# Kernel tuning notes

Hardware: AMD Instinct MI355X
Metric: run time of the kernel (lower is better)

Reference implementation:

```python
import jax, jax.numpy as jnp
import numpy as np

B, CIN, COUT, H, W, HEADS = 8, 128, 128, 256, 256, 32
CI = COUT // HEADS  # channels per head


def setup_inputs() -> dict:
    key = jax.random.key(0)
    ks = jax.random.split(key, 6)
    s_in = (2.0 / CIN) ** 0.5
    s_mid = (2.0 / COUT) ** 0.5
    return {
        "u": jax.random.normal(ks[0], (B, CIN, H, W), jnp.float32),
        "w_f1": jax.random.normal(ks[1], (COUT, CIN), jnp.float32) * s_in,
        "b_f1": jnp.zeros((COUT,), jnp.float32),
        # small flow weights -> small displacements (realistic warping)
        "w_f2": jax.random.normal(ks[2], (2 * HEADS, COUT), jnp.float32) * 0.02 * s_mid,
        "b_f2": jnp.zeros((2 * HEADS,), jnp.float32),
        "w_v": jax.random.normal(ks[3], (COUT, CIN), jnp.float32) * s_in,
        "b_v": jnp.zeros((COUT,), jnp.float32),
    }


def _conv1x1(x, w, b):
    # x: (B, Cin, H, W), w: (Cout, Cin) -> (B, Cout, H, W)
    return jnp.einsum('bchw,oc->bohw', x, w) + b[None, :, None, None]


def _periodic_bilinear(v, grid):
    """grid_sample, bilinear, align_corners=False, periodic in both H and W.
    Equivalent to custom_grid_sample2d with padding_modes=('periodic','periodic'):
    pixel coords are wrapped mod size and the (i+1) neighbor wraps to index 0
    (the torch code pads with the first row/col and samples with border mode).
    v: (N, C, H, W); grid: (N, H, W, 2) with [...,0]=x, [...,1]=y in [-1,1].
    """
    N, C, Hi, Wi = v.shape
    gx, gy = grid[..., 0], grid[..., 1]
    # unnormalize (align_corners=False) then wrap periodically
    px = jnp.mod(((gx + 1.0) * Wi - 1.0) * 0.5, Wi)
    py = jnp.mod(((gy + 1.0) * Hi - 1.0) * 0.5, Hi)
    x0 = jnp.floor(px)
    y0 = jnp.floor(py)
    wx = px - x0
    wy = py - y0
    x0i = jnp.clip(x0.astype(jnp.int32), 0, Wi - 1)
    y0i = jnp.clip(y0.astype(jnp.int32), 0, Hi - 1)
    x1i = jnp.mod(x0i + 1, Wi)
    y1i = jnp.mod(y0i + 1, Hi)
    vf = v.reshape(N, C, Hi * Wi)

    def gather(yi, xi):
        idx = (yi * Wi + xi).reshape(N, 1, Hi * Wi)
        return jnp.take_along_axis(vf, idx, axis=2).reshape(N, C, Hi, Wi)

    w00 = ((1.0 - wx) * (1.0 - wy))[:, None]
    w01 = (wx * (1.0 - wy))[:, None]
    w10 = ((1.0 - wx) * wy)[:, None]
    w11 = (wx * wy)[:, None]
    return (gather(y0i, x0i) * w00 + gather(y0i, x1i) * w01
            + gather(y1i, x0i) * w10 + gather(y1i, x1i) * w11)


def _base_grid(Hi, Wi):
    # create_grid: stack(meshgrid[::-1]) -> [...,0]=x (varies along W), [...,1]=y
    yy, xx = jnp.meshgrid(jnp.linspace(-1.0, 1.0, Hi),
                          jnp.linspace(-1.0, 1.0, Wi), indexing='ij')
    return jnp.stack([xx, yy], axis=-1)  # (H, W, 2)


def reference(u, w_f1, b_f1, w_f2, b_f2, w_v, b_v):
    Bq = u.shape[0]
    # flow_head: conv1x1 -> relu -> conv1x1
    hmid = jax.nn.relu(_conv1x1(u, w_f1, b_f1))
    flow = _conv1x1(hmid, w_f2, b_f2)          # (B, heads*2, H, W)
    value = _conv1x1(u, w_v, b_v)              # (B, Cout, H, W)
    # rearrange 'B (heads dir) H W -> (B heads) H W dir'
    flow = flow.reshape(Bq, HEADS, 2, H, W).transpose(0, 1, 3, 4, 2)
    flow = flow.reshape(Bq * HEADS, H, W, 2)
    grid = _base_grid(H, W)[None] + flow       # warp: x + delta(x)
    # rearrange 'B (heads C_i) H W -> (B heads) C_i H W'
    vh = value.reshape(Bq * HEADS, CI, H, W)
    out = _periodic_bilinear(vh, grid)
    # '(B heads) C_i H W -> B (heads C_i) H W'
    return out.reshape(Bq, COUT, H, W)
```

## Files before the change

### kernel.cpp

```cpp
#include <hip/hip_runtime.h>
#include <hip/hip_fp16.h>


typedef unsigned short u16;
typedef unsigned int   u32;
using short8   = __attribute__((ext_vector_type(8))) short;
using f32x4    = __attribute__((ext_vector_type(4))) float;
using ushort4v = __attribute__((ext_vector_type(4))) unsigned short;

#define HW     65536
#define NTILES 8192

__device__ __forceinline__ u16 f2h(float f) {
  return __half_as_ushort(__float2half(f));
}
__device__ __forceinline__ float h2f(u16 h) {
  return __half2float(__ushort_as_half(h));
}

#define BAR_LGKM() do {                                      \
    asm volatile("s_waitcnt lgkmcnt(0)" ::: "memory");       \
    __builtin_amdgcn_s_barrier();                            \
    asm volatile("" ::: "memory");                           \
  } while (0)

__device__ __forceinline__ short8 frag_from_f32(const float* __restrict__ src) {
  float4 a = *(const float4*)src;
  float4 b = *(const float4*)(src + 4);
  short8 r;
  r[0] = (short)f2h(a.x); r[1] = (short)f2h(a.y);
  r[2] = (short)f2h(a.z); r[3] = (short)f2h(a.w);
  r[4] = (short)f2h(b.x); r[5] = (short)f2h(b.y);
  r[6] = (short)f2h(b.z); r[7] = (short)f2h(b.w);
  return r;
}

__device__ __forceinline__ void vf_load_tile(const float* __restrict__ u,
                                             int tile, int tid,
                                             float* __restrict__ r) {
  const int gbase = tile << 6;
  const float* ub = u + ((size_t)(gbase >> 16) << 23) + (gbase & 65535);
  const int p  = tid & 63;
  const int cb = (tid >> 6) << 3;
#pragma unroll
  for (int pass = 0; pass < 4; ++pass)
#pragma unroll
    for (int j = 0; j < 8; ++j)
      r[pass * 8 + j] = ub[(size_t)(cb + pass * 32 + j) * HW + p];
}

__device__ __forceinline__ void vf_write_tile(u16* __restrict__ buf, int tid,
                                              const float* __restrict__ r) {
  const int p  = tid & 63;
  const int cb = (tid >> 6) << 3;
#pragma unroll
  for (int pass = 0; pass < 4; ++pass) {
    int c0 = cb + pass * 32;
    uint4 pk;
    pk.x = (u32)f2h(r[pass * 8 + 0]) | ((u32)f2h(r[pass * 8 + 1]) << 16);
    pk.y = (u32)f2h(r[pass * 8 + 2]) | ((u32)f2h(r[pass * 8 + 3]) << 16);
    pk.z = (u32)f2h(r[pass * 8 + 4]) | ((u32)f2h(r[pass * 8 + 5]) << 16);
    pk.w = (u32)f2h(r[pass * 8 + 6]) | ((u32)f2h(r[pass * 8 + 7]) << 16);
    *(uint4*)((char*)buf + p * 256 + (((c0 >> 3) ^ (p & 15)) << 4)) = pk;
  }
}

__global__ __launch_bounds__(256, 2) void vf_kernel(
    const float* __restrict__ u,  const float* __restrict__ w1,
    const float* __restrict__ b1, const float* __restrict__ w2,
    const float* __restrict__ b2, const float* __restrict__ wv,
    const float* __restrict__ bv, u16* __restrict__ vout,
    u32* __restrict__ fout)
{
  __shared__ u16 t_lds[2][64 * 128];

  const int tid  = threadIdx.x;
  const int lane = tid & 63;
  const int w    = tid >> 6;
  const int m15  = lane & 15;
  const int q    = lane >> 4;

  short8 w1f[2][4], wvf[2][4], w2f[4];
#pragma unroll
  for (int nt = 0; nt < 2; ++nt)
#pragma unroll
    for (int kc = 0; kc < 4; ++kc) {
      const int row = w * 32 + nt * 16 + m15;
      w1f[nt][kc] = frag_from_f32(w1 + row * 128 + kc * 32 + q * 8);
      wvf[nt][kc] = frag_from_f32(wv + row * 128 + kc * 32 + q * 8);
    }
#pragma unroll
  for (int kc = 0; kc < 4; ++kc)
    w2f[kc] = frag_from_f32(w2 + (w * 16 + m15) * 128 + kc * 32 + q * 8);

  f32x4 vbias[2], hbias[2], fbias;
#pragma unroll
  for (int nt = 0; nt < 2; ++nt) {
    vbias[nt] = *(const f32x4*)(bv + w * 32 + nt * 16 + q * 4);
    hbias[nt] = *(const f32x4*)(b1 + w * 32 + nt * 16 + q * 4);
  }
  fbias = *(const f32x4*)(b2 + w * 16 + q * 4);

  const int step = (int)gridDim.x;
  int tile = blockIdx.x;
  float sreg[32];

  vf_load_tile(u, tile, tid, sreg);
  vf_write_tile(t_lds[0], tid, sreg);
  BAR_LGKM();

  int cur = 0;
  for (; tile < NTILES; ) {
    const int gbase = tile << 6;
    const int b     = gbase >> 16;
    const int img   = gbase & 65535;
    const int nxt   = tile + step;
    const bool have_next = (nxt < NTILES);

    if (have_next) vf_load_tile(u, nxt, tid, sreg);

    f32x4 zero = {0.f, 0.f, 0.f, 0.f};
    f32x4 hm[2][4], va[2][4];
#pragma unroll
    for (int nt = 0; nt < 2; ++nt)
#pragma unroll
      for (int pxb = 0; pxb < 4; ++pxb) { hm[nt][pxb] = zero; va[nt][pxb] = zero; }

#pragma unroll
    for (int kc = 0; kc < 4; ++kc) {
      short8 uf[4];
#pragma unroll
      for (int pxb = 0; pxb < 4; ++pxb)
        uf[pxb] = *(const short8*)((const char*)t_lds[cur] +
                                   (pxb * 16 + m15) * 256 +
                                   ((((kc << 2) + q) ^ m15) << 4));
#pragma unroll
      for (int pxb = 0; pxb < 4; ++pxb)
#pragma unroll
        for (int nt = 0; nt < 2; ++nt) {
          hm[nt][pxb] = __builtin_amdgcn_mfma_f32_16x16x32_f16(
              w1f[nt][kc], uf[pxb], hm[nt][pxb], 0, 0, 0);
          va[nt][pxb] = __builtin_amdgcn_mfma_f32_16x16x32_f16(
              wvf[nt][kc], uf[pxb], va[nt][pxb], 0, 0, 0);
        }
    }
    BAR_LGKM();

#pragma unroll
    for (int nt = 0; nt < 2; ++nt) {
      const int ch0   = w * 32 + nt * 16 + q * 4;
      const int chunk = ch0 >> 3;
      const int inner = (ch0 & 7) << 1;
#pragma unroll
      for (int pxb = 0; pxb < 4; ++pxb) {
        const int px = pxb * 16 + m15;
        float h0 = fmaxf(hm[nt][pxb][0] + hbias[nt][0], 0.f);
        float h1 = fmaxf(hm[nt][pxb][1] + hbias[nt][1], 0.f);
        float h2 = fmaxf(hm[nt][pxb][2] + hbias[nt][2], 0.f);
        float h3 = fmaxf(hm[nt][pxb][3] + hbias[nt][3], 0.f);
        uint2 pk;
        pk.x = (u32)f2h(h0) | ((u32)f2h(h1) << 16);
        pk.y = (u32)f2h(h2) | ((u32)f2h(h3) << 16);
        *(uint2*)((char*)t_lds[cur] + px * 256 + ((chunk ^ (px & 15)) << 4) +
                  inner) = pk;
      }
    }

#pragma unroll
    for (int nt = 0; nt < 2; ++nt) {
      const int head = w * 8 + nt * 4 + q;
#pragma unroll
      for (int pxb = 0; pxb < 4; ++pxb) {
        f32x4 v = va[nt][pxb];
        uint2 pk;
        pk.x = (u32)f2h(v[0] + vbias[nt][0]) | ((u32)f2h(v[1] + vbias[nt][1]) << 16);
        pk.y = (u32)f2h(v[2] + vbias[nt][2]) | ((u32)f2h(v[3] + vbias[nt][3]) << 16);
        *(uint2*)(vout + ((((size_t)(b * 32 + head)) << 16) + img +
                          pxb * 16 + m15) * 4) = pk;
      }
    }
    BAR_LGKM();

    f32x4 fl[4];
#pragma unroll
    for (int pxb = 0; pxb < 4; ++pxb) fl[pxb] = zero;
#pragma unroll
    for (int kc = 0; kc < 4; ++kc)
#pragma unroll
      for (int pxb = 0; pxb < 4; ++pxb) {
        short8 hf = *(const short8*)((const char*)t_lds[cur] +
                                     (pxb * 16 + m15) * 256 +
                                     ((((kc << 2) + q) ^ m15) << 4));
        fl[pxb] = __builtin_amdgcn_mfma_f32_16x16x32_f16(
            w2f[kc], hf, fl[pxb], 0, 0, 0);
      }

#pragma unroll
    for (int pxb = 0; pxb < 4; ++pxb) {
      f32x4 v = fl[pxb];
      const int h0 = w * 8 + q * 2;
      u32 pa = (u32)f2h(v[0] + fbias[0]) | ((u32)f2h(v[1] + fbias[1]) << 16);
      u32 pb = (u32)f2h(v[2] + fbias[2]) | ((u32)f2h(v[3] + fbias[3]) << 16);
      u32* fp = fout + (((size_t)(b * 32 + h0)) << 16) + img + pxb * 16 + m15;
      fp[0]  = pa;
      fp[HW] = pb;
    }

    if (have_next) vf_write_tile(t_lds[cur ^ 1], tid, sreg);
    BAR_LGKM();
    cur ^= 1;
    tile = nxt;
  }
}

__global__ __launch_bounds__(256) void warp_kernel(
    const u16* __restrict__ value, const u32* __restrict__ flow,
    float* __restrict__ out)
{
  const int P   = blockIdx.x;
  const int L   = ((P & 7) << 11) | (P >> 3);
  const int hb  = L >> 6;
  const int g   = L & 63;
  const int col = threadIdx.x;

  const u16* vb = value + ((size_t)hb << 18);
  const u32* fp = flow + ((size_t)hb << 16) + (g << 10) + col;

  u32 f[4];
#pragma unroll
  for (int r = 0; r < 4; ++r) f[r] = fp[r << 8];

  float w00[4], w01[4], w10[4], w11[4];
  ushort4v t00[4], t01[4], t10[4], t11[4];
#pragma unroll
  for (int r = 0; r < 4; ++r) {
    float fx = h2f((u16)(f[r] & 0xffffu));
    float fy = h2f((u16)(f[r] >> 16));
    const int hq = (g << 2) + r;
    float gx = -1.f + (2.f / 255.f) * (float)col + fx;
    float gy = -1.f + (2.f / 255.f) * (float)hq + fy;
    float pxr = ((gx + 1.f) * 256.f - 1.f) * 0.5f;
    float pyr = ((gy + 1.f) * 256.f - 1.f) * 0.5f;
    float px = pxr - floorf(pxr * (1.f / 256.f)) * 256.f;
    float py = pyr - floorf(pyr * (1.f / 256.f)) * 256.f;
    if (px >= 256.f) px -= 256.f;
    if (py >= 256.f) py -= 256.f;
    if (px < 0.f) px = 0.f;
    if (py < 0.f) py = 0.f;
    float x0f = floorf(px), y0f = floorf(py);
    float wx = px - x0f, wy = py - y0f;
    int x0 = (int)x0f; if (x0 > 255) x0 = 255;
    int y0 = (int)y0f; if (y0 > 255) y0 = 255;
    int x1 = (x0 + 1) & 255;
    int y1 = (y0 + 1) & 255;
    w00[r] = (1.f - wx) * (1.f - wy);
    w01[r] = wx * (1.f - wy);
    w10[r] = (1.f - wx) * wy;
    w11[r] = wx * wy;
    t00[r] = *(const ushort4v*)(vb + ((y0 * 256 + x0) << 2));
    t01[r] = *(const ushort4v*)(vb + ((y0 * 256 + x1) << 2));
    t10[r] = *(const ushort4v*)(vb + ((y1 * 256 + x0) << 2));
    t11[r] = *(const ushort4v*)(vb + ((y1 * 256 + x1) << 2));
  }

  float* ob = out + ((size_t)hb << 18) + (g << 10) + col;
#pragma unroll
  for (int r = 0; r < 4; ++r)
#pragma unroll
    for (int ci = 0; ci < 4; ++ci) {
      float res = w00[r] * h2f(t00[r][ci]) + w01[r] * h2f(t01[r][ci])
                + w10[r] * h2f(t10[r][ci]) + w11[r] * h2f(t11[r][ci]);
      __builtin_nontemporal_store(res, ob + (r << 8) + ((size_t)ci << 16));
    }
}

extern "C" void kernel_launch(void* const* d_in, const int* in_sizes, int n_in,
                              void* d_out, int out_size, void* d_ws, size_t ws_size,
                              hipStream_t stream) {
  const float* u  = (const float*)d_in[0];
  const float* w1 = (const float*)d_in[1];
  const float* b1 = (const float*)d_in[2];
  const float* w2 = (const float*)d_in[3];
  const float* b2 = (const float*)d_in[4];
  const float* wv = (const float*)d_in[5];
  const float* bv = (const float*)d_in[6];

  u16* value_ws = (u16*)d_ws;
  u32* flow_ws  = (u32*)((char*)d_ws + 134217728);
  float* out    = (float*)d_out;

  vf_kernel<<<dim3(512), dim3(256), 0, stream>>>(u, w1, b1, w2, b2, wv, bv,
                                                 value_ws, flow_ws);
  warp_kernel<<<dim3(16384), dim3(256), 0, stream>>>(value_ws, flow_ws, out);
}
```

Before: 766.7 us.

## Stream input tiles via global_load_lds double buffer and coarsen warp kernel rows

The value/flow kernel now prefetches the next input tile straight into an fp32 LDS double buffer with global_load_lds. It then converts that buffer to an fp16 tile in a separate step, which frees the 32 staging registers and takes the global-load latency off the register path. The warp kernel now handles 8 rows per block instead of 4, in two batches of gathers, and folds the grid unnormalization into one fma. The cost is more LDS per block, which may limit occupancy, and an extra barrier per tile.

```diff
diff --git a/kernel.cpp b/kernel.cpp
--- a/kernel.cpp
+++ b/kernel.cpp
@@ -35,33 +35,38 @@
   return r;
 }
 
-__device__ __forceinline__ void vf_load_tile(const float* __restrict__ u,
-                                             int tile, int tid,
-                                             float* __restrict__ r) {
+__device__ __forceinline__ void vf_issue_tile(const float* __restrict__ u,
+                                              int tile, int tid,
+                                              float* __restrict__ sbuf) {
   const int gbase = tile << 6;
-  const float* ub = u + ((size_t)(gbase >> 16) << 23) + (gbase & 65535);
+  const int wave  = tid >> 6;
+  const int lane  = tid & 63;
+  const float* ub = u + ((size_t)(gbase >> 16) << 23) + (gbase & 65535)
+                      + (size_t)(lane >> 4) * HW + ((lane & 15) << 2);
+#pragma unroll
+  for (int i = 0; i < 8; ++i) {
+    const int ch0 = wave * 32 + i * 4;
+    __builtin_amdgcn_global_load_lds(
+        (const __attribute__((address_space(1))) void*)(ub + (size_t)ch0 * HW),
+        (__attribute__((address_space(3))) void*)(sbuf + ch0 * 64),
+        16, 0, 0);
+  }
+}
+
+__device__ __forceinline__ void vf_convert(const float* __restrict__ sbuf,
+                                           u16* __restrict__ T, int tid) {
   const int p  = tid & 63;
   const int cb = (tid >> 6) << 3;
 #pragma unroll
-  for (int pass = 0; pass < 4; ++pass)
-#pragma unroll
-    for (int j = 0; j < 8; ++j)
-      r[pass * 8 + j] = ub[(size_t)(cb + pass * 32 + j) * HW + p];
-}
-
-__device__ __forceinline__ void vf_write_tile(u16* __restrict__ buf, int tid,
-                                              const float* __restrict__ r) {
-  const int p  = tid & 63;
-  const int cb = (tid >> 6) << 3;
-#pragma unroll
   for (int pass = 0; pass < 4; ++pass) {
-    int c0 = cb + pass * 32;
+    const int c0 = cb + pass * 32;
+    const float* rp = sbuf + c0 * 64 + p;
     uint4 pk;
-    pk.x = (u32)f2h(r[pass * 8 + 0]) | ((u32)f2h(r[pass * 8 + 1]) << 16);
-    pk.y = (u32)f2h(r[pass * 8 + 2]) | ((u32)f2h(r[pass * 8 + 3]) << 16);
-    pk.z = (u32)f2h(r[pass * 8 + 4]) | ((u32)f2h(r[pass * 8 + 5]) << 16);
-    pk.w = (u32)f2h(r[pass * 8 + 6]) | ((u32)f2h(r[pass * 8 + 7]) << 16);
-    *(uint4*)((char*)buf + p * 256 + (((c0 >> 3) ^ (p & 15)) << 4)) = pk;
+    pk.x = (u32)f2h(rp[0])   | ((u32)f2h(rp[64])  << 16);
+    pk.y = (u32)f2h(rp[128]) | ((u32)f2h(rp[192]) << 16);
+    pk.z = (u32)f2h(rp[256]) | ((u32)f2h(rp[320]) << 16);
+    pk.w = (u32)f2h(rp[384]) | ((u32)f2h(rp[448]) << 16);
+    *(uint4*)((char*)T + p * 256 + (((c0 >> 3) ^ (p & 15)) << 4)) = pk;
   }
 }
 
@@ -72,7 +77,8 @@
     const float* __restrict__ bv, u16* __restrict__ vout,
     u32* __restrict__ fout)
 {
-  __shared__ u16 t_lds[2][64 * 128];
+  __shared__ float S[2][128 * 64];
+  __shared__ u16   T[64 * 128];
 
   const int tid  = threadIdx.x;
   const int lane = tid & 63;
@@ -102,22 +108,30 @@
   fbias = *(const f32x4*)(b2 + w * 16 + q * 4);
 
   const int step = (int)gridDim.x;
-  int tile = blockIdx.x;
-  float sreg[32];
-
-  vf_load_tile(u, tile, tid, sreg);
-  vf_write_tile(t_lds[0], tid, sreg);
-  BAR_LGKM();
-
-  int cur = 0;
-  for (; tile < NTILES; ) {
+  float* Sc = &S[0][0];
+  float* Sn = &S[1][0];
+
+  vf_issue_tile(u, blockIdx.x, tid, Sc);
+
+  for (int tile = blockIdx.x; tile < NTILES; tile += step) {
     const int gbase = tile << 6;
     const int b     = gbase >> 16;
     const int img   = gbase & 65535;
     const int nxt   = tile + step;
     const bool have_next = (nxt < NTILES);
 
-    if (have_next) vf_load_tile(u, nxt, tid, sreg);
+    if (have_next) vf_issue_tile(u, nxt, tid, Sn);
+
+    if (have_next) {
+      asm volatile("s_waitcnt vmcnt(8)" ::: "memory");
+    } else {
+      asm volatile("s_waitcnt vmcnt(0)" ::: "memory");
+    }
+    __builtin_amdgcn_s_barrier();
+    __builtin_amdgcn_sched_barrier(0);
+
+    vf_convert(Sc, T, tid);
+    BAR_LGKM();
 
     f32x4 zero = {0.f, 0.f, 0.f, 0.f};
     f32x4 hm[2][4], va[2][4];
@@ -131,8 +145,7 @@
       short8 uf[4];
 #pragma unroll
       for (int pxb = 0; pxb < 4; ++pxb)
-        uf[pxb] = *(const short8*)((const char*)t_lds[cur] +
-                                   (pxb * 16 + m15) * 256 +
+        uf[pxb] = *(const short8*)((const char*)T + (pxb * 16 + m15) * 256 +
                                    ((((kc << 2) + q) ^ m15) << 4));
 #pragma unroll
       for (int pxb = 0; pxb < 4; ++pxb)
@@ -161,8 +174,7 @@
         uint2 pk;
         pk.x = (u32)f2h(h0) | ((u32)f2h(h1) << 16);
         pk.y = (u32)f2h(h2) | ((u32)f2h(h3) << 16);
-        *(uint2*)((char*)t_lds[cur] + px * 256 + ((chunk ^ (px & 15)) << 4) +
-                  inner) = pk;
+        *(uint2*)((char*)T + px * 256 + ((chunk ^ (px & 15)) << 4) + inner) = pk;
       }
     }
 
@@ -188,8 +200,7 @@
     for (int kc = 0; kc < 4; ++kc)
 #pragma unroll
       for (int pxb = 0; pxb < 4; ++pxb) {
-        short8 hf = *(const short8*)((const char*)t_lds[cur] +
-                                     (pxb * 16 + m15) * 256 +
+        short8 hf = *(const short8*)((const char*)T + (pxb * 16 + m15) * 256 +
                                      ((((kc << 2) + q) ^ m15) << 4));
         fl[pxb] = __builtin_amdgcn_mfma_f32_16x16x32_f16(
             w2f[kc], hf, fl[pxb], 0, 0, 0);
@@ -206,10 +217,7 @@
       fp[HW] = pb;
     }
 
-    if (have_next) vf_write_tile(t_lds[cur ^ 1], tid, sreg);
-    BAR_LGKM();
-    cur ^= 1;
-    tile = nxt;
+    float* t = Sc; Sc = Sn; Sn = t;
   }
 }
 
@@ -218,60 +226,65 @@
     float* __restrict__ out)
 {
   const int P   = blockIdx.x;
-  const int L   = ((P & 7) << 11) | (P >> 3);
-  const int hb  = L >> 6;
-  const int g   = L & 63;
+  const int L   = ((P & 7) << 10) | (P >> 3);
+  const int hb  = L >> 5;
+  const int g   = L & 31;
   const int col = threadIdx.x;
 
   const u16* vb = value + ((size_t)hb << 18);
-  const u32* fp = flow + ((size_t)hb << 16) + (g << 10) + col;
-
-  u32 f[4];
-#pragma unroll
-  for (int r = 0; r < 4; ++r) f[r] = fp[r << 8];
-
-  float w00[4], w01[4], w10[4], w11[4];
-  ushort4v t00[4], t01[4], t10[4], t11[4];
-#pragma unroll
-  for (int r = 0; r < 4; ++r) {
-    float fx = h2f((u16)(f[r] & 0xffffu));
-    float fy = h2f((u16)(f[r] >> 16));
-    const int hq = (g << 2) + r;
-    float gx = -1.f + (2.f / 255.f) * (float)col + fx;
-    float gy = -1.f + (2.f / 255.f) * (float)hq + fy;
-    float pxr = ((gx + 1.f) * 256.f - 1.f) * 0.5f;
-    float pyr = ((gy + 1.f) * 256.f - 1.f) * 0.5f;
-    float px = pxr - floorf(pxr * (1.f / 256.f)) * 256.f;
-    float py = pyr - floorf(pyr * (1.f / 256.f)) * 256.f;
-    if (px >= 256.f) px -= 256.f;
-    if (py >= 256.f) py -= 256.f;
-    if (px < 0.f) px = 0.f;
-    if (py < 0.f) py = 0.f;
-    float x0f = floorf(px), y0f = floorf(py);
-    float wx = px - x0f, wy = py - y0f;
-    int x0 = (int)x0f; if (x0 > 255) x0 = 255;
-    int y0 = (int)y0f; if (y0 > 255) y0 = 255;
-    int x1 = (x0 + 1) & 255;
-    int y1 = (y0 + 1) & 255;
-    w00[r] = (1.f - wx) * (1.f - wy);
-    w01[r] = wx * (1.f - wy);
-    w10[r] = (1.f - wx) * wy;
-    w11[r] = wx * wy;
-    t00[r] = *(const ushort4v*)(vb + ((y0 * 256 + x0) << 2));
-    t01[r] = *(const ushort4v*)(vb + ((y0 * 256 + x1) << 2));
-    t10[r] = *(const ushort4v*)(vb + ((y1 * 256 + x0) << 2));
-    t11[r] = *(const ushort4v*)(vb + ((y1 * 256 + x1) << 2));
-  }
-
-  float* ob = out + ((size_t)hb << 18) + (g << 10) + col;
-#pragma unroll
-  for (int r = 0; r < 4; ++r)
-#pragma unroll
-    for (int ci = 0; ci < 4; ++ci) {
-      float res = w00[r] * h2f(t00[r][ci]) + w01[r] * h2f(t01[r][ci])
-                + w10[r] * h2f(t10[r][ci]) + w11[r] * h2f(t11[r][ci]);
-      __builtin_nontemporal_store(res, ob + (r << 8) + ((size_t)ci << 16));
-    }
+  const u32* fp = flow + ((size_t)hb << 16) + (g << 11) + col;
+
+  u32 f[8];
+#pragma unroll
+  for (int r = 0; r < 8; ++r) f[r] = fp[r << 8];
+
+  const float cbase = (float)col * (256.f / 255.f) - 0.5f;
+  float* ob = out + ((size_t)hb << 18) + (g << 11) + col;
+
+#pragma unroll
+  for (int half = 0; half < 2; ++half) {
+    float w00[4], w01[4], w10[4], w11[4];
+    ushort4v t00[4], t01[4], t10[4], t11[4];
+#pragma unroll
+    for (int j = 0; j < 4; ++j) {
+      const int r  = half * 4 + j;
+      const int hq = (g << 3) + r;
+      float fx = h2f((u16)(f[r] & 0xffffu));
+      float fy = h2f((u16)(f[r] >> 16));
+      float pxr = fmaf(fx, 128.f, cbase);
+      float pyr = fmaf(fy, 128.f, (float)hq * (256.f / 255.f) - 0.5f);
+      float px = pxr - floorf(pxr * (1.f / 256.f)) * 256.f;
+      float py = pyr - floorf(pyr * (1.f / 256.f)) * 256.f;
+      if (px >= 256.f) px -= 256.f;
+      if (py >= 256.f) py -= 256.f;
+      if (px < 0.f) px = 0.f;
+      if (py < 0.f) py = 0.f;
+      float x0f = floorf(px), y0f = floorf(py);
+      float wx = px - x0f, wy = py - y0f;
+      int x0 = (int)x0f; if (x0 > 255) x0 = 255;
+      int y0 = (int)y0f; if (y0 > 255) y0 = 255;
+      int x1 = (x0 + 1) & 255;
+      int y1 = (y0 + 1) & 255;
+      w00[j] = (1.f - wx) * (1.f - wy);
+      w01[j] = wx * (1.f - wy);
+      w10[j] = (1.f - wx) * wy;
+      w11[j] = wx * wy;
+      t00[j] = *(const ushort4v*)(vb + ((y0 * 256 + x0) << 2));
+      t01[j] = *(const ushort4v*)(vb + ((y0 * 256 + x1) << 2));
+      t10[j] = *(const ushort4v*)(vb + ((y1 * 256 + x0) << 2));
+      t11[j] = *(const ushort4v*)(vb + ((y1 * 256 + x1) << 2));
+    }
+#pragma unroll
+    for (int j = 0; j < 4; ++j) {
+      const int r = half * 4 + j;
+#pragma unroll
+      for (int ci = 0; ci < 4; ++ci) {
+        float res = w00[j] * h2f(t00[j][ci]) + w01[j] * h2f(t01[j][ci])
+                  + w10[j] * h2f(t10[j][ci]) + w11[j] * h2f(t11[j][ci]);
+        __builtin_nontemporal_store(res, ob + (r << 8) + ((size_t)ci << 16));
+      }
+    }
+  }
 }
 
 extern "C" void kernel_launch(void* const* d_in, const int* in_sizes, int n_in,
@@ -291,5 +304,5 @@
 
   vf_kernel<<<dim3(512), dim3(256), 0, stream>>>(u, w1, b1, w2, b2, wv, bv,
                                                  value_ws, flow_ws);
-  warp_kernel<<<dim3(16384), dim3(256), 0, stream>>>(value_ws, flow_ws, out);
-}
+  warp_kernel<<<dim3(8192), dim3(256), 0, stream>>>(value_ws, flow_ws, out);
+}
```

After: 623.5 us. 18.7% less time.
